# Optimization experiments

Measured on AMD Instinct MI355X. Metric: run time of the kernel, lower is better.

Reference implementation:

```python
import jax, jax.numpy as jnp
import numpy as np

B, LS, VS = 4, 1024, 1024
VH, LH, H = 1024, 1024, 16
HD = LH // H  # head_dim = 64


def setup_inputs() -> dict:
    key = jax.random.key(0)
    ks = jax.random.split(key, 10)
    s = 0.02
    return {
        "v_hidden_states": jax.random.normal(ks[0], (B, VS, VH), jnp.float32),
        "l_hidden_states": jax.random.normal(ks[1], (B, LS, LH), jnp.float32),
        "q_w": jax.random.normal(ks[2], (LH, LH), jnp.float32) * s,
        "q_b": jnp.zeros((LH,), jnp.float32),
        "k_w": jax.random.normal(ks[3], (VH, LH), jnp.float32) * s,
        "k_b": jnp.zeros((LH,), jnp.float32),
        "v_w": jax.random.normal(ks[4], (VH, LH), jnp.float32) * s,
        "v_b": jnp.zeros((LH,), jnp.float32),
        "o_w": jax.random.normal(ks[5], (LH, LH), jnp.float32) * s,
        "o_b": jnp.zeros((LH,), jnp.float32),
    }


def reference(v_hidden_states, l_hidden_states, q_w, q_b, k_w, k_b, v_w, v_b, o_w, o_b):
    b, ls, _ = l_hidden_states.shape
    vs = v_hidden_states.shape[1]
    q = (l_hidden_states @ q_w + q_b).reshape(b, ls, H, HD)
    k = (v_hidden_states @ k_w + k_b).reshape(b, vs, H, HD)
    v = (v_hidden_states @ v_w + v_b).reshape(b, vs, H, HD)
    # NOTE: original scales by sqrt(hidden_size), not sqrt(head_dim)
    scale = jnp.sqrt(jnp.asarray(LH, q.dtype))
    scores = jnp.einsum("blhd,bvhd->bhlv", q, k) / scale
    attn = jax.nn.softmax(scores, axis=-1)
    out = jnp.einsum("bhlv,bvhd->blhd", attn, v).reshape(b, ls, LH)
    return out @ o_w + o_b
```

## Files before the change

kernel.cpp:

```cpp
#include <hip/hip_runtime.h>

typedef __bf16 bf16;
typedef __attribute__((ext_vector_type(4))) __bf16 bf16x4;
typedef __attribute__((ext_vector_type(8))) __bf16 bf16x8;
typedef __attribute__((ext_vector_type(4))) float f32x4;

static __device__ __forceinline__ f32x4 mfma_16x16x32(bf16x8 a, bf16x8 b, f32x4 c) {
    return __builtin_amdgcn_mfma_f32_16x16x32_bf16(a, b, c, 0, 0, 0);
}

static __device__ __forceinline__ bf16x8 load8(const float* p) {
    f32x4 a = *(const f32x4*)p;
    f32x4 b = *(const f32x4*)(p + 4);
    bf16x8 r;
    r[0] = (bf16)a[0]; r[1] = (bf16)a[1]; r[2] = (bf16)a[2]; r[3] = (bf16)a[3];
    r[4] = (bf16)b[0]; r[5] = (bf16)b[1]; r[6] = (bf16)b[2]; r[7] = (bf16)b[3];
    return r;
}

static __device__ __forceinline__ void gload_lds16(const void* g, void* l) {
    __builtin_amdgcn_global_load_lds(
        (const __attribute__((address_space(1))) void*)g,
        (__attribute__((address_space(3))) void*)l, 16, 0, 0);
}

#define QSCALE 0.0450842200277801f

__global__ __launch_bounds__(256) void prep_kernel(
    const float* __restrict__ l_h, const float* __restrict__ v_h,
    const float* __restrict__ w0, const float* __restrict__ w1,
    const float* __restrict__ w2, const float* __restrict__ w3,
    bf16* __restrict__ l_bf, bf16* __restrict__ v_bf,
    bf16* __restrict__ dq, bf16* __restrict__ dkv, bf16* __restrict__ dov)
{
    const int id = blockIdx.x;
    if (id < 4096) {
        const float* s = (id < 2048) ? l_h : v_h;
        bf16*       d = (id < 2048) ? l_bf : v_bf;
        const int   bb = (id < 2048) ? id : id - 2048;
        const size_t i = ((size_t)bb * 256 + threadIdx.x) * 8;
        *(bf16x8*)(d + i) = load8(s + i);
        return;
    }
    const int widx = id - 4096;
    const int z    = widx >> 8;
    const int rem  = widx & 255;
    const int j0   = (rem & 15) * 64;
    const int i0   = (rem >> 4) * 64;
    const float* src; bf16* dst;
    switch (z) {
        case 0:  src = w0; dst = dq; break;
        case 1:  src = w1; dst = dkv; break;
        case 2:  src = w2; dst = dkv + (size_t)1024 * 1024; break;
        default: src = w3; dst = dov; break;
    }
    const float wscale = (z == 0) ? QSCALE : 1.0f;
    __shared__ float T[64][65];
    const int tx = threadIdx.x & 15;
    const int ty = threadIdx.x >> 4;
    #pragma unroll
    for (int it = 0; it < 4; ++it) {
        f32x4 v = *(const f32x4*)(src + (size_t)(i0 + ty + it * 16) * 1024 + j0 + tx * 4);
        T[ty + it * 16][tx * 4 + 0] = v[0];
        T[ty + it * 16][tx * 4 + 1] = v[1];
        T[ty + it * 16][tx * 4 + 2] = v[2];
        T[ty + it * 16][tx * 4 + 3] = v[3];
    }
    __syncthreads();
    #pragma unroll
    for (int it = 0; it < 4; ++it) {
        const int jj = ty + it * 16;
        bf16x4 o;
        o[0] = (bf16)(T[tx * 4 + 0][jj] * wscale);
        o[1] = (bf16)(T[tx * 4 + 1][jj] * wscale);
        o[2] = (bf16)(T[tx * 4 + 2][jj] * wscale);
        o[3] = (bf16)(T[tx * 4 + 3][jj] * wscale);
        *(bf16x4*)(dst + (size_t)(j0 + jj) * 1024 + i0 + tx * 4) = o;
    }
}

__global__ __launch_bounds__(256, 3) void proj128_kernel(
    const bf16* __restrict__ l_bf, const bf16* __restrict__ v_bf,
    const bf16* __restrict__ QWt,  const bf16* __restrict__ KVWt,
    const float* __restrict__ q_b, const float* __restrict__ k_b,
    const float* __restrict__ v_b,
    bf16* __restrict__ Qh, bf16* __restrict__ Kh, bf16* __restrict__ Vt)
{
    __shared__ __align__(16) bf16 As[2][128][32];
    __shared__ __align__(16) bf16 Bs[2][128][32];

    const int t    = threadIdx.x;
    const int lane = t & 63;
    const int wave = t >> 6;
    const int wm   = wave & 1;
    const int wn   = wave >> 1;
    const int l15  = lane & 15;
    const int quad = lane >> 4;

    const bool isQ = blockIdx.x < 8;
    const bf16* A  = isQ ? l_bf : v_bf;
    const bf16* Bt = isQ ? QWt  : KVWt;
    const int  gn0 = (isQ ? blockIdx.x : blockIdx.x - 8) * 128;
    const int  gm0 = blockIdx.y * 128;
    const int  K   = 1024;

    const int srow    = lane >> 2;
    const int chunk_g = (lane & 3) ^ ((srow >> 1) & 3);
    const size_t aoff = (size_t)(gm0 + wave * 32 + srow) * K + chunk_g * 8;
    const size_t boff = (size_t)(gn0 + wave * 32 + srow) * K + chunk_g * 8;

    f32x4 acc[4][4];
    #pragma unroll
    for (int i = 0; i < 4; ++i)
        #pragma unroll
        for (int j = 0; j < 4; ++j)
            acc[i][j] = (f32x4){0.f, 0.f, 0.f, 0.f};

    #define PSTAGE(k0_, buf_)                                                      \
        {                                                                          \
            _Pragma("unroll")                                                      \
            for (int q = 0; q < 2; ++q) {                                          \
                gload_lds16(A  + aoff + (size_t)q * 16 * K + (k0_),                \
                            &As[buf_][wave * 32 + q * 16][0]);                     \
                gload_lds16(Bt + boff + (size_t)q * 16 * K + (k0_),                \
                            &Bs[buf_][wave * 32 + q * 16][0]);                     \
            }                                                                      \
        }

    PSTAGE(0, 0);
    __syncthreads();

    for (int k0 = 0; k0 < K; k0 += 32) {
        const int buf = (k0 >> 5) & 1;
        if (k0 + 32 < K) PSTAGE(k0 + 32, buf ^ 1);

        bf16x8 af[4], bfr[4];
        #pragma unroll
        for (int mt = 0; mt < 4; ++mt) {
            const int row = wm * 64 + mt * 16 + l15;
            af[mt] = *(const bf16x8*)(&As[buf][row][(quad ^ ((row >> 1) & 3)) * 8]);
        }
        #pragma unroll
        for (int nt = 0; nt < 4; ++nt) {
            const int row = wn * 64 + nt * 16 + l15;
            bfr[nt] = *(const bf16x8*)(&Bs[buf][row][(quad ^ ((row >> 1) & 3)) * 8]);
        }
        #pragma unroll
        for (int mt = 0; mt < 4; ++mt)
            #pragma unroll
            for (int nt = 0; nt < 4; ++nt)
                acc[mt][nt] = mfma_16x16x32(af[mt], bfr[nt], acc[mt][nt]);

        __syncthreads();
    }
    #undef PSTAGE

    #pragma unroll
    for (int nt = 0; nt < 4; ++nt) {
        const int col = gn0 + wn * 64 + nt * 16 + l15;
        float bb; bf16* dst; bool hm;
        if (isQ)             { bb = q_b[col] * QSCALE;   dst = Qh; hm = true;  }
        else if (col < 1024) { bb = k_b[col];            dst = Kh; hm = true;  }
        else                 { bb = v_b[col - 1024];     dst = Vt; hm = false; }
        #pragma unroll
        for (int mt = 0; mt < 4; ++mt) {
            #pragma unroll
            for (int r = 0; r < 4; ++r) {
                const int row = gm0 + wm * 64 + mt * 16 + quad * 4 + r;
                const float v = acc[mt][nt][r] + bb;
                if (hm) {
                    const size_t idx =
                        ((size_t)((row >> 10) * 16 + (col >> 6)) * 1024 +
                         (row & 1023)) * 64 + (col & 63);
                    dst[idx] = (bf16)v;
                } else {
                    const int vc = col - 1024;
                    const size_t idx =
                        ((size_t)((row >> 10) * 16 + (vc >> 6)) * 64 +
                         (vc & 63)) * 1024 + (row & 1023);
                    dst[idx] = (bf16)v;
                }
            }
        }
    }
}

static __device__ __forceinline__ void gemm_core_128x64(
    const bf16* __restrict__ A, const bf16* __restrict__ Bt, int K,
    int gm0, int gn0, bf16 (*As)[128][32], bf16 (*Bs)[64][32], f32x4 acc[4][2])
{
    const int t    = threadIdx.x;
    const int lane = t & 63;
    const int wave = t >> 6;
    const int wm   = wave & 1;
    const int wn   = wave >> 1;
    const int l15  = lane & 15;
    const int quad = lane >> 4;

    const int srow    = lane >> 2;
    const int chunk_g = (lane & 3) ^ ((srow >> 1) & 3);
    const size_t aoff = (size_t)(gm0 + wave * 32 + srow) * K + chunk_g * 8;
    const size_t boff = (size_t)(gn0 + wave * 16 + srow) * K + chunk_g * 8;

    #pragma unroll
    for (int i = 0; i < 4; ++i)
        #pragma unroll
        for (int j = 0; j < 2; ++j)
            acc[i][j] = (f32x4){0.f, 0.f, 0.f, 0.f};

    #define OSTAGE(k0_, buf_)                                                     \
        {                                                                         \
            gload_lds16(A + aoff + (k0_),                  &As[buf_][wave * 32][0]);       \
            gload_lds16(A + aoff + (size_t)16 * K + (k0_), &As[buf_][wave * 32 + 16][0]);  \
            gload_lds16(Bt + boff + (k0_),                 &Bs[buf_][wave * 16][0]);       \
        }

    OSTAGE(0, 0);
    __syncthreads();

    for (int k0 = 0; k0 < K; k0 += 32) {
        const int buf = (k0 >> 5) & 1;
        if (k0 + 32 < K) OSTAGE(k0 + 32, buf ^ 1);

        bf16x8 af[4], bfr[2];
        #pragma unroll
        for (int mt = 0; mt < 4; ++mt) {
            const int row = wm * 64 + mt * 16 + l15;
            af[mt] = *(const bf16x8*)(&As[buf][row][(quad ^ ((row >> 1) & 3)) * 8]);
        }
        #pragma unroll
        for (int nt = 0; nt < 2; ++nt) {
            const int row = wn * 32 + nt * 16 + l15;
            bfr[nt] = *(const bf16x8*)(&Bs[buf][row][(quad ^ ((row >> 1) & 3)) * 8]);
        }
        #pragma unroll
        for (int mt = 0; mt < 4; ++mt)
            #pragma unroll
            for (int nt = 0; nt < 2; ++nt)
                acc[mt][nt] = mfma_16x16x32(af[mt], bfr[nt], acc[mt][nt]);

        __syncthreads();
    }
    #undef OSTAGE
}

__global__ __launch_bounds__(256, 3) void ogemm_kernel(
    const bf16* __restrict__ Aw, const bf16* __restrict__ OWt,
    const float* __restrict__ o_b, float* __restrict__ C)
{
    __shared__ __align__(16) bf16 As[2][128][32];
    __shared__ __align__(16) bf16 Bs[2][64][32];

    const int gn0 = blockIdx.x * 64;
    const int gm0 = blockIdx.y * 128;

    f32x4 acc[4][2];
    gemm_core_128x64(Aw, OWt, 1024, gm0, gn0, As, Bs, acc);

    const int lane = threadIdx.x & 63;
    const int wave = threadIdx.x >> 6;
    const int wm   = wave & 1;
    const int wn   = wave >> 1;
    const int l15  = lane & 15;
    const int quad = lane >> 4;

    #pragma unroll
    for (int nt = 0; nt < 2; ++nt) {
        const int col = gn0 + wn * 32 + nt * 16 + l15;
        const float bb = o_b[col];
        #pragma unroll
        for (int mt = 0; mt < 4; ++mt) {
            #pragma unroll
            for (int r = 0; r < 4; ++r) {
                const int row = gm0 + wm * 64 + mt * 16 + quad * 4 + r;
                C[(size_t)row * 1024 + col] = acc[mt][nt][r] + bb;
            }
        }
    }
}

__global__ __launch_bounds__(256) void attn_kernel(
    const bf16* __restrict__ Q, const bf16* __restrict__ K,
    const bf16* __restrict__ V, bf16* __restrict__ O)
{
    const int t    = threadIdx.x;
    const int lane = t & 63;
    const int wave = t >> 6;
    const int l15  = lane & 15;
    const int quad = lane >> 4;

    const int head = blockIdx.x;
    const int q0   = blockIdx.y * 128;
    const int b    = head >> 4;
    const int h    = head & 15;

    __shared__ __align__(16) bf16 Kb[2][64][64];
    __shared__ __align__(16) bf16 Vb[2][64][64];
    __shared__ __align__(16) bf16 P[4][32][72];

    const bf16* Qp  = Q + ((size_t)head * 1024 + q0 + wave * 32) * 64;
    const bf16* Kp  = K + (size_t)head * 1024 * 64;
    const bf16* Vtp = V + (size_t)head * 64 * 1024;

    const int r8  = lane >> 3;
    const int c8  = lane & 7;
    const int swz = (c8 ^ r8) * 8;

    bf16x8 aq[2][2];
    #pragma unroll
    for (int mt = 0; mt < 2; ++mt)
        #pragma unroll
        for (int kc = 0; kc < 2; ++kc)
            aq[mt][kc] = *(const bf16x8*)(Qp + (mt * 16 + l15) * 64 + kc * 32 + quad * 8);

    bf16x8 vones;
    #pragma unroll
    for (int j = 0; j < 8; ++j) vones[j] = (bf16)1.0f;

    f32x4 oacc[2][4];
    #pragma unroll
    for (int mt = 0; mt < 2; ++mt)
        #pragma unroll
        for (int nt = 0; nt < 4; ++nt)
            oacc[mt][nt] = (f32x4){0.f, 0.f, 0.f, 0.f};
    f32x4 lacc[2];
    lacc[0] = (f32x4){0.f, 0.f, 0.f, 0.f};
    lacc[1] = (f32x4){0.f, 0.f, 0.f, 0.f};

    #define STAGE(c, buf)                                                          \
        {                                                                          \
            const int kv0_ = (c) * 64;                                             \
            _Pragma("unroll")                                                      \
            for (int g = 0; g < 2; ++g) {                                          \
                const int R = wave * 16 + g * 8;                                   \
                gload_lds16(Kp + (size_t)(kv0_ + R + r8) * 64 + swz,               \
                            &Kb[buf][R][0]);                                       \
                gload_lds16(Vtp + (size_t)(R + r8) * 1024 + kv0_ + swz,            \
                            &Vb[buf][R][0]);                                       \
            }                                                                      \
        }

    STAGE(0, 0);

    const int sw = l15 & 7;

    for (int c = 0; c < 16; ++c) {
        const int buf = c & 1;
        __syncthreads();
        if (c + 1 < 16) STAGE(c + 1, buf ^ 1);

        #pragma unroll
        for (int nt = 0; nt < 4; ++nt) {
            const bf16* krow = &Kb[buf][nt * 16 + l15][0];
            bf16x8 bk0 = *(const bf16x8*)(krow + (quad ^ sw) * 8);
            bf16x8 bk1 = *(const bf16x8*)(krow + ((quad + 4) ^ sw) * 8);
            #pragma unroll
            for (int mt = 0; mt < 2; ++mt) {
                f32x4 s = (f32x4){0.f, 0.f, 0.f, 0.f};
                s = mfma_16x16x32(aq[mt][0], bk0, s);
                s = mfma_16x16x32(aq[mt][1], bk1, s);
                #pragma unroll
                for (int r = 0; r < 4; ++r) {
                    const float e = __builtin_amdgcn_exp2f(s[r]);
                    P[wave][mt * 16 + quad * 4 + r][nt * 16 + l15] = (bf16)e;
                }
            }
        }

        #pragma unroll
        for (int mt = 0; mt < 2; ++mt) {
            bf16x8 pa0 = *(const bf16x8*)(&P[wave][mt * 16 + l15][quad * 8]);
            bf16x8 pa1 = *(const bf16x8*)(&P[wave][mt * 16 + l15][32 + quad * 8]);
            lacc[mt] = mfma_16x16x32(pa0, vones, lacc[mt]);
            lacc[mt] = mfma_16x16x32(pa1, vones, lacc[mt]);
            #pragma unroll
            for (int nt = 0; nt < 4; ++nt) {
                const bf16* vrow = &Vb[buf][nt * 16 + l15][0];
                bf16x8 bv0 = *(const bf16x8*)(vrow + (quad ^ sw) * 8);
                bf16x8 bv1 = *(const bf16x8*)(vrow + ((quad + 4) ^ sw) * 8);
                oacc[mt][nt] = mfma_16x16x32(pa0, bv0, oacc[mt][nt]);
                oacc[mt][nt] = mfma_16x16x32(pa1, bv1, oacc[mt][nt]);
            }
        }
    }
    #undef STAGE

    #pragma unroll
    for (int mt = 0; mt < 2; ++mt) {
        const float invs[4] = {1.0f / lacc[mt][0], 1.0f / lacc[mt][1],
                               1.0f / lacc[mt][2], 1.0f / lacc[mt][3]};
        #pragma unroll
        for (int nt = 0; nt < 4; ++nt) {
            #pragma unroll
            for (int r = 0; r < 4; ++r) {
                const int row = q0 + wave * 32 + mt * 16 + quad * 4 + r;
                O[((size_t)b * 1024 + row) * 1024 + h * 64 + nt * 16 + l15] =
                    (bf16)(oacc[mt][nt][r] * invs[r]);
            }
        }
    }
}

extern "C" void kernel_launch(void* const* d_in, const int* in_sizes, int n_in,
                              void* d_out, int out_size, void* d_ws, size_t ws_size,
                              hipStream_t stream)
{
    const float* v_h = (const float*)d_in[0];
    const float* l_h = (const float*)d_in[1];
    const float* q_w = (const float*)d_in[2];
    const float* q_b = (const float*)d_in[3];
    const float* k_w = (const float*)d_in[4];
    const float* k_b = (const float*)d_in[5];
    const float* v_w = (const float*)d_in[6];
    const float* v_b = (const float*)d_in[7];
    const float* o_w = (const float*)d_in[8];
    const float* o_b = (const float*)d_in[9];
    float* out = (float*)d_out;

    const size_t SZ = (size_t)4096 * 1024;
    const size_t WZ = (size_t)1024 * 1024;

    bf16* l_bf = (bf16*)d_ws;
    bf16* v_bf = l_bf + SZ;
    bf16* QWt  = v_bf + SZ;
    bf16* KVWt = QWt + WZ;
    bf16* OWt  = KVWt + 2 * WZ;
    bf16* Qh   = OWt + WZ;
    bf16* Kh   = Qh + SZ;
    bf16* Vt   = Kh + SZ;
    bf16* Aw   = Vt + SZ;

    prep_kernel<<<dim3(5120), 256, 0, stream>>>(
        l_h, v_h, q_w, k_w, v_w, o_w, l_bf, v_bf, QWt, KVWt, OWt);

    proj128_kernel<<<dim3(24, 32), 256, 0, stream>>>(
        l_bf, v_bf, QWt, KVWt, q_b, k_b, v_b, Qh, Kh, Vt);

    attn_kernel<<<dim3(64, 8), 256, 0, stream>>>(Qh, Kh, Vt, Aw);

    ogemm_kernel<<<dim3(16, 32), 256, 0, stream>>>(Aw, OWt, o_b, out);

    (void)in_sizes; (void)n_in; (void)out_size; (void)ws_size;
}
```

Baseline: 200.7 us.

## Triple-buffer projection and output GEMMs with split barriers and XCD-aware block remap

Switches the Q/KV projection GEMM and the output GEMM from double to triple-buffered LDS staging with a two-tile prefetch distance. The single __syncthreads per step becomes a vmcnt wait plus barrier before compute and an lgkmcnt wait plus barrier after it. MFMA sections now run at raised wave priority. Block indices are remapped so consecutive tiles land on the same XCD, aiming for better L2 reuse. The cost is more LDS per block, which may cut occupancy under launch_bounds(256,3), and hand-counted vmcnt values that must match the number of loads issued.

```diff
diff --git a/kernel.cpp b/kernel.cpp
--- a/kernel.cpp
+++ b/kernel.cpp
@@ -25,6 +25,20 @@
 }
 
 #define QSCALE 0.0450842200277801f
+
+#define SYNC_PRE(N)                                                      \
+    do {                                                                 \
+        asm volatile("s_waitcnt vmcnt(" #N ")" ::: "memory");            \
+        __builtin_amdgcn_s_barrier();                                    \
+        __builtin_amdgcn_sched_barrier(0);                               \
+    } while (0)
+
+#define SYNC_POST()                                                     \
+    do {                                                                \
+        asm volatile("s_waitcnt lgkmcnt(0)" ::: "memory");              \
+        __builtin_amdgcn_sched_barrier(0);                              \
+        __builtin_amdgcn_s_barrier();                                   \
+    } while (0)
 
 __global__ __launch_bounds__(256) void prep_kernel(
     const float* __restrict__ l_h, const float* __restrict__ v_h,
@@ -86,8 +100,8 @@
     const float* __restrict__ v_b,
     bf16* __restrict__ Qh, bf16* __restrict__ Kh, bf16* __restrict__ Vt)
 {
-    __shared__ __align__(16) bf16 As[2][128][32];
-    __shared__ __align__(16) bf16 Bs[2][128][32];
+    __shared__ __align__(16) bf16 As[3][128][32];
+    __shared__ __align__(16) bf16 Bs[3][128][32];
 
     const int t    = threadIdx.x;
     const int lane = t & 63;
@@ -97,11 +111,16 @@
     const int l15  = lane & 15;
     const int quad = lane >> 4;
 
-    const bool isQ = blockIdx.x < 8;
+    const int orig = blockIdx.y * 24 + blockIdx.x;
+    const int wg   = (orig & 7) * 96 + (orig >> 3);
+    const int by   = wg / 24;
+    const int bx   = wg - by * 24;
+
+    const bool isQ = bx < 8;
     const bf16* A  = isQ ? l_bf : v_bf;
     const bf16* Bt = isQ ? QWt  : KVWt;
-    const int  gn0 = (isQ ? blockIdx.x : blockIdx.x - 8) * 128;
-    const int  gm0 = blockIdx.y * 128;
+    const int  gn0 = (isQ ? bx : bx - 8) * 128;
+    const int  gm0 = by * 128;
     const int  K   = 1024;
 
     const int srow    = lane >> 2;
@@ -127,33 +146,50 @@
             }                                                                      \
         }
 
+    #define PCOMPUTE(bufi)                                                         \
+        {                                                                          \
+            bf16x8 af[4], bfr[4];                                                  \
+            _Pragma("unroll")                                                      \
+            for (int mt = 0; mt < 4; ++mt) {                                       \
+                const int row = wm * 64 + mt * 16 + l15;                           \
+                af[mt] = *(const bf16x8*)(&As[bufi][row][(quad ^ ((row >> 1) & 3)) * 8]); \
+            }                                                                      \
+            _Pragma("unroll")                                                      \
+            for (int nt = 0; nt < 4; ++nt) {                                       \
+                const int row = wn * 64 + nt * 16 + l15;                           \
+                bfr[nt] = *(const bf16x8*)(&Bs[bufi][row][(quad ^ ((row >> 1) & 3)) * 8]); \
+            }                                                                      \
+            __builtin_amdgcn_s_setprio(1);                                         \
+            _Pragma("unroll")                                                      \
+            for (int mt = 0; mt < 4; ++mt)                                         \
+                _Pragma("unroll")                                                  \
+                for (int nt = 0; nt < 4; ++nt)                                     \
+                    acc[mt][nt] = mfma_16x16x32(af[mt], bfr[nt], acc[mt][nt]);     \
+            __builtin_amdgcn_s_setprio(0);                                         \
+        }
+
     PSTAGE(0, 0);
-    __syncthreads();
-
-    for (int k0 = 0; k0 < K; k0 += 32) {
-        const int buf = (k0 >> 5) & 1;
-        if (k0 + 32 < K) PSTAGE(k0 + 32, buf ^ 1);
-
-        bf16x8 af[4], bfr[4];
-        #pragma unroll
-        for (int mt = 0; mt < 4; ++mt) {
-            const int row = wm * 64 + mt * 16 + l15;
-            af[mt] = *(const bf16x8*)(&As[buf][row][(quad ^ ((row >> 1) & 3)) * 8]);
-        }
-        #pragma unroll
-        for (int nt = 0; nt < 4; ++nt) {
-            const int row = wn * 64 + nt * 16 + l15;
-            bfr[nt] = *(const bf16x8*)(&Bs[buf][row][(quad ^ ((row >> 1) & 3)) * 8]);
-        }
-        #pragma unroll
-        for (int mt = 0; mt < 4; ++mt)
-            #pragma unroll
-            for (int nt = 0; nt < 4; ++nt)
-                acc[mt][nt] = mfma_16x16x32(af[mt], bfr[nt], acc[mt][nt]);
-
-        __syncthreads();
-    }
+    PSTAGE(32, 1);
+    int bc = 0, bn2 = 2;
+
+    for (int k0 = 0; k0 < K - 64; k0 += 32) {
+        PSTAGE(k0 + 64, bn2);
+        SYNC_PRE(8);
+        PCOMPUTE(bc);
+        SYNC_POST();
+        int nb = bc + 1;  if (nb == 3) nb = 0;
+        int nn = bn2 + 1; if (nn == 3) nn = 0;
+        bc = nb; bn2 = nn;
+    }
+    SYNC_PRE(4);
+    PCOMPUTE(bc);
+    SYNC_POST();
+    bc = (bc + 1 == 3) ? 0 : bc + 1;
+    SYNC_PRE(0);
+    PCOMPUTE(bc);
+
     #undef PSTAGE
+    #undef PCOMPUTE
 
     #pragma unroll
     for (int nt = 0; nt < 4; ++nt) {
@@ -185,10 +221,13 @@
     }
 }
 
-static __device__ __forceinline__ void gemm_core_128x64(
-    const bf16* __restrict__ A, const bf16* __restrict__ Bt, int K,
-    int gm0, int gn0, bf16 (*As)[128][32], bf16 (*Bs)[64][32], f32x4 acc[4][2])
+__global__ __launch_bounds__(256, 3) void ogemm_kernel(
+    const bf16* __restrict__ Aw, const bf16* __restrict__ OWt,
+    const float* __restrict__ o_b, float* __restrict__ C)
 {
+    __shared__ __align__(16) bf16 As[3][128][32];
+    __shared__ __align__(16) bf16 Bs[3][64][32];
+
     const int t    = threadIdx.x;
     const int lane = t & 63;
     const int wave = t >> 6;
@@ -197,72 +236,78 @@
     const int l15  = lane & 15;
     const int quad = lane >> 4;
 
+    const int orig = blockIdx.y * 16 + blockIdx.x;
+    const int wg   = (orig & 7) * 64 + (orig >> 3);
+    const int by   = wg >> 4;
+    const int bx   = wg & 15;
+
+    const int gn0 = bx * 64;
+    const int gm0 = by * 128;
+    const int K   = 1024;
+
     const int srow    = lane >> 2;
     const int chunk_g = (lane & 3) ^ ((srow >> 1) & 3);
     const size_t aoff = (size_t)(gm0 + wave * 32 + srow) * K + chunk_g * 8;
     const size_t boff = (size_t)(gn0 + wave * 16 + srow) * K + chunk_g * 8;
 
+    f32x4 acc[4][2];
     #pragma unroll
     for (int i = 0; i < 4; ++i)
         #pragma unroll
         for (int j = 0; j < 2; ++j)
             acc[i][j] = (f32x4){0.f, 0.f, 0.f, 0.f};
 
-    #define OSTAGE(k0_, buf_)                                                     \
-        {                                                                         \
-            gload_lds16(A + aoff + (k0_),                  &As[buf_][wave * 32][0]);       \
-            gload_lds16(A + aoff + (size_t)16 * K + (k0_), &As[buf_][wave * 32 + 16][0]);  \
-            gload_lds16(Bt + boff + (k0_),                 &Bs[buf_][wave * 16][0]);       \
+    #define OSTAGE(k0_, buf_)                                                          \
+        {                                                                              \
+            gload_lds16(Aw + aoff + (k0_),                  &As[buf_][wave * 32][0]);  \
+            gload_lds16(Aw + aoff + (size_t)16 * K + (k0_), &As[buf_][wave * 32 + 16][0]); \
+            gload_lds16(OWt + boff + (k0_),                 &Bs[buf_][wave * 16][0]);  \
+        }
+
+    #define OCOMPUTE(bufi)                                                             \
+        {                                                                              \
+            bf16x8 af[4], bfr[2];                                                      \
+            _Pragma("unroll")                                                          \
+            for (int mt = 0; mt < 4; ++mt) {                                           \
+                const int row = wm * 64 + mt * 16 + l15;                               \
+                af[mt] = *(const bf16x8*)(&As[bufi][row][(quad ^ ((row >> 1) & 3)) * 8]); \
+            }                                                                          \
+            _Pragma("unroll")                                                          \
+            for (int nt = 0; nt < 2; ++nt) {                                           \
+                const int row = wn * 32 + nt * 16 + l15;                               \
+                bfr[nt] = *(const bf16x8*)(&Bs[bufi][row][(quad ^ ((row >> 1) & 3)) * 8]); \
+            }                                                                          \
+            __builtin_amdgcn_s_setprio(1);                                             \
+            _Pragma("unroll")                                                          \
+            for (int mt = 0; mt < 4; ++mt)                                             \
+                _Pragma("unroll")                                                      \
+                for (int nt = 0; nt < 2; ++nt)                                         \
+                    acc[mt][nt] = mfma_16x16x32(af[mt], bfr[nt], acc[mt][nt]);         \
+            __builtin_amdgcn_s_setprio(0);                                             \
         }
 
     OSTAGE(0, 0);
-    __syncthreads();
-
-    for (int k0 = 0; k0 < K; k0 += 32) {
-        const int buf = (k0 >> 5) & 1;
-        if (k0 + 32 < K) OSTAGE(k0 + 32, buf ^ 1);
-
-        bf16x8 af[4], bfr[2];
-        #pragma unroll
-        for (int mt = 0; mt < 4; ++mt) {
-            const int row = wm * 64 + mt * 16 + l15;
-            af[mt] = *(const bf16x8*)(&As[buf][row][(quad ^ ((row >> 1) & 3)) * 8]);
-        }
-        #pragma unroll
-        for (int nt = 0; nt < 2; ++nt) {
-            const int row = wn * 32 + nt * 16 + l15;
-            bfr[nt] = *(const bf16x8*)(&Bs[buf][row][(quad ^ ((row >> 1) & 3)) * 8]);
-        }
-        #pragma unroll
-        for (int mt = 0; mt < 4; ++mt)
-            #pragma unroll
-            for (int nt = 0; nt < 2; ++nt)
-                acc[mt][nt] = mfma_16x16x32(af[mt], bfr[nt], acc[mt][nt]);
-
-        __syncthreads();
-    }
+    OSTAGE(32, 1);
+    int bc = 0, bn2 = 2;
+
+    for (int k0 = 0; k0 < K - 64; k0 += 32) {
+        OSTAGE(k0 + 64, bn2);
+        SYNC_PRE(6);
+        OCOMPUTE(bc);
+        SYNC_POST();
+        int nb = bc + 1;  if (nb == 3) nb = 0;
+        int nn = bn2 + 1; if (nn == 3) nn = 0;
+        bc = nb; bn2 = nn;
+    }
+    SYNC_PRE(3);
+    OCOMPUTE(bc);
+    SYNC_POST();
+    bc = (bc + 1 == 3) ? 0 : bc + 1;
+    SYNC_PRE(0);
+    OCOMPUTE(bc);
+
     #undef OSTAGE
-}
-
-__global__ __launch_bounds__(256, 3) void ogemm_kernel(
-    const bf16* __restrict__ Aw, const bf16* __restrict__ OWt,
-    const float* __restrict__ o_b, float* __restrict__ C)
-{
-    __shared__ __align__(16) bf16 As[2][128][32];
-    __shared__ __align__(16) bf16 Bs[2][64][32];
-
-    const int gn0 = blockIdx.x * 64;
-    const int gm0 = blockIdx.y * 128;
-
-    f32x4 acc[4][2];
-    gemm_core_128x64(Aw, OWt, 1024, gm0, gn0, As, Bs, acc);
-
-    const int lane = threadIdx.x & 63;
-    const int wave = threadIdx.x >> 6;
-    const int wm   = wave & 1;
-    const int wn   = wave >> 1;
-    const int l15  = lane & 15;
-    const int quad = lane >> 4;
+    #undef OCOMPUTE
 
     #pragma unroll
     for (int nt = 0; nt < 2; ++nt) {
```

Result: faster. 189.8 us, median of 3 (-5.5%).
